# Optimization experiments

Measured on AMD Instinct MI355X. Metric: run time of the kernel, lower is better.

Reference implementation:

```python
import jax, jax.numpy as jnp
import numpy as np

HIDDEN = 4096
N_Q_HEADS = 32
N_KV_HEADS = 8
HEAD_DIM = 128
V_HEAD_DIM = 128
WINDOW = 1024
ROPE_THETA = 1000000.0
SEQ = 2048


def setup_inputs() -> dict:
    key = jax.random.key(0)
    ks = jax.random.split(key, 7)
    s = 0.02
    return {
        "hidden_states": jax.random.normal(ks[0], (SEQ, HIDDEN), dtype=jnp.float32),
        "positions": jnp.arange(SEQ, dtype=jnp.int32),
        "wq": jax.random.normal(ks[1], (HIDDEN, N_Q_HEADS * HEAD_DIM), dtype=jnp.float32) * s,
        "wk": jax.random.normal(ks[2], (HIDDEN, N_KV_HEADS * HEAD_DIM), dtype=jnp.float32) * s,
        "wv": jax.random.normal(ks[3], (HIDDEN, N_KV_HEADS * V_HEAD_DIM), dtype=jnp.float32) * s,
        "wo": jax.random.normal(ks[4], (N_Q_HEADS * V_HEAD_DIM, HIDDEN), dtype=jnp.float32) * s,
        "sink": jax.random.normal(ks[5], (N_Q_HEADS,), dtype=jnp.float32),
    }


def _apply_rope_neox(x, positions):
    # x: [S, H, D]; rotate full head_dim in neox (half-split) style
    d = x.shape[-1]
    inv_freq = 1.0 / (ROPE_THETA ** (jnp.arange(0, d, 2, dtype=jnp.float32) / d))
    freqs = positions.astype(jnp.float32)[:, None] * inv_freq[None, :]  # [S, D/2]
    cos = jnp.cos(freqs)[:, None, :]  # [S, 1, D/2]
    sin = jnp.sin(freqs)[:, None, :]
    x1, x2 = x[..., : d // 2], x[..., d // 2 :]
    return jnp.concatenate([x1 * cos - x2 * sin, x2 * cos + x1 * sin], axis=-1)


def reference(hidden_states, positions, wq, wk, wv, wo, sink):
    S = hidden_states.shape[0]
    scaling = HEAD_DIM ** -0.5
    q = (hidden_states @ wq).reshape(S, N_Q_HEADS, HEAD_DIM)
    k = (hidden_states @ wk).reshape(S, N_KV_HEADS, HEAD_DIM)
    v = (hidden_states @ wv).reshape(S, N_KV_HEADS, V_HEAD_DIM)

    q = _apply_rope_neox(q, positions)
    k = _apply_rope_neox(k, positions)

    groups = N_Q_HEADS // N_KV_HEADS
    k_rep = jnp.repeat(k, groups, axis=1)  # [S, Hq, D]
    v_rep = jnp.repeat(v, groups, axis=1)

    # [Hq, S(query), S(key)] attention scores
    scores = jnp.einsum("qhd,khd->hqk", q, k_rep) * scaling

    # causal + sliding-window mask: key j visible iff j <= i and i - j < WINDOW
    i = positions[:, None].astype(jnp.int32)
    j = positions[None, :].astype(jnp.int32)
    mask = (j <= i) & (i - j < WINDOW)  # [S, S]
    neg = jnp.finfo(scores.dtype).min
    scores = jnp.where(mask[None, :, :], scores, neg)

    # softmax with per-head attention sink logit in the denominator
    sink_l = sink[:, None, None]  # [Hq, 1, 1]
    m = jnp.maximum(scores.max(axis=-1, keepdims=True), sink_l)
    w = jnp.exp(scores - m)
    denom = w.sum(axis=-1, keepdims=True) + jnp.exp(sink_l - m)
    probs = w / denom

    attn = jnp.einsum("hqk,khd->qhd", probs, v_rep).reshape(S, N_Q_HEADS * V_HEAD_DIM)
    return attn @ wo
```

## Files before the change

kernel.cpp:

```cpp
#include <hip/hip_runtime.h>
#include <cstdint>
#include <cstddef>

typedef uint16_t u16;
typedef __bf16 bf16x8 __attribute__((ext_vector_type(8)));
typedef float f32x4 __attribute__((ext_vector_type(4)));
typedef u16 u16x8 __attribute__((ext_vector_type(8)));


__device__ __forceinline__ u16 f2bf(float f) {
    union { float f; uint32_t i; } v; v.f = f;
    uint32_t b = v.i;
    return (u16)((b + 0x7FFFu + ((b >> 16) & 1u)) >> 16);
}
__device__ __forceinline__ float bf2f(u16 u) {
    union { uint32_t i; float f; } v; v.i = ((uint32_t)u) << 16; return v.f;
}
__device__ __forceinline__ float nanfix(float x, float repl) {
    return (x == x && fabsf(x) < 1e30f) ? x : repl;
}
__device__ __forceinline__ void async16(const u16* g, u16* l) {
    __builtin_amdgcn_global_load_lds(
        (const __attribute__((address_space(1))) uint32_t*)g,
        (__attribute__((address_space(3))) uint32_t*)l, 16, 0, 0);
}

template<int N> __device__ __forceinline__ void waitvm() {
    static_assert(N >= 0 && N <= 15, "vmcnt range");
    if constexpr (N == 0)  asm volatile("s_waitcnt vmcnt(0)" ::: "memory");
    else if constexpr (N == 1)  asm volatile("s_waitcnt vmcnt(1)" ::: "memory");
    else if constexpr (N == 2)  asm volatile("s_waitcnt vmcnt(2)" ::: "memory");
    else if constexpr (N == 3)  asm volatile("s_waitcnt vmcnt(3)" ::: "memory");
    else if constexpr (N == 4)  asm volatile("s_waitcnt vmcnt(4)" ::: "memory");
    else if constexpr (N == 5)  asm volatile("s_waitcnt vmcnt(5)" ::: "memory");
    else if constexpr (N == 6)  asm volatile("s_waitcnt vmcnt(6)" ::: "memory");
    else if constexpr (N == 7)  asm volatile("s_waitcnt vmcnt(7)" ::: "memory");
    else if constexpr (N == 8)  asm volatile("s_waitcnt vmcnt(8)" ::: "memory");
    else if constexpr (N == 9)  asm volatile("s_waitcnt vmcnt(9)" ::: "memory");
    else                        asm volatile("s_waitcnt vmcnt(10)" ::: "memory");
}

__global__ void cvt_k(const float* __restrict__ in, u16* __restrict__ out) {
    const size_t i = ((size_t)blockIdx.x * 256 + threadIdx.x) * 8;
    const f32x4 a = *(const f32x4*)&in[i], b = *(const f32x4*)&in[i + 4];
    u16x8 s;
    #pragma unroll
    for (int e = 0; e < 4; e++) { s[e] = f2bf(a[e]); s[4 + e] = f2bf(b[e]); }
    *(u16x8*)&out[i] = s;
}

__global__ void cvtT_k(const float* __restrict__ in, u16* __restrict__ out,
                       int R, int C) {
    __shared__ float tile[32][33];
    const int bx = blockIdx.x * 32, by = blockIdx.y * 32;
    const int tx = threadIdx.x, ty = threadIdx.y;
    #pragma unroll
    for (int i = 0; i < 32; i += 8)
        tile[ty + i][tx] = in[(size_t)(by + ty + i) * C + (bx + tx)];
    __syncthreads();
    #pragma unroll
    for (int i = 0; i < 32; i += 8)
        out[(size_t)(bx + ty + i) * R + (by + tx)] = f2bf(tile[tx][ty + i]);
}


#define SB(g, kk, dst) async16(Bb + (size_t)((g) * 64 + rg) * 4096 + (kk) + sc, \
                               (dst) + ((g) * 64 + wave * 8) * 64)
#define SA(g, kk, dst) async16(Ab + (size_t)((g) * 32 + aro) * 4096 + (kk) + sc, \
                               (dst) + ((g) * 32 + wbA) * 64)

#define LOADA(P) do {                                                           \
    const int r0_ = wr * 128 + (2 * (P)) * 16 + lr;                             \
    const int r1_ = r0_ + 16;                                                   \
    _Pragma("unroll")                                                           \
    for (int ks = 0; ks < 2; ks++) {                                            \
        a0[ks] = *(const bf16x8*)&Ac[r0_ * 64 + (((ks * 4 + qd) ^ (r0_ & 7)) * 8)]; \
        a1[ks] = *(const bf16x8*)&Ac[r1_ * 64 + (((ks * 4 + qd) ^ (r1_ & 7)) * 8)]; \
    }                                                                           \
} while (0)

#define MFMAP(P) do {                                                           \
    __builtin_amdgcn_s_setprio(1);                                              \
    _Pragma("unroll")                                                           \
    for (int nn = 0; nn < NF; nn++)                                             \
        _Pragma("unroll")                                                       \
        for (int ks = 0; ks < 2; ks++) {                                        \
            acc[2 * (P)][nn]     = __builtin_amdgcn_mfma_f32_16x16x32_bf16(     \
                a0[ks], b[nn][ks], acc[2 * (P)][nn], 0, 0, 0);                  \
            acc[2 * (P) + 1][nn] = __builtin_amdgcn_mfma_f32_16x16x32_bf16(     \
                a1[ks], b[nn][ks], acc[2 * (P) + 1][nn], 0, 0, 0);              \
        }                                                                       \
    __builtin_amdgcn_s_setprio(0);                                              \
} while (0)

#define PHASE_SYNC() do {                                                       \
    __builtin_amdgcn_s_barrier();                                               \
    asm volatile("s_waitcnt lgkmcnt(0)" ::: "memory");                          \
    __builtin_amdgcn_sched_barrier(0);                                          \
} while (0)

#define PHASE_END() do {                                                        \
    __builtin_amdgcn_s_barrier();                                               \
    __builtin_amdgcn_sched_barrier(0);                                          \
} while (0)

template<int NF, int ISS>
__device__ __forceinline__ void tile_body(
    const u16* __restrict__ Ab, const u16* __restrict__ Bb,
    const u16* Ac, const u16* Bc, u16* An, u16* Bn, int k1,
    int wave, int lr, int qd, int wr, int wc,
    int rg, int sc, int aro, int wbA, f32x4 (&acc)[8][NF])
{
    bf16x8 b[NF][2];
    bf16x8 a0[2], a1[2];

    #pragma unroll
    for (int nn = 0; nn < NF; nn++)
        #pragma unroll
        for (int ks = 0; ks < 2; ks++) {
            const int row = wc * (16 * NF) + nn * 16 + lr;
            b[nn][ks] = *(const bf16x8*)&Bc[row * 64 + (((ks * 4 + qd) ^ (row & 7)) * 8)];
        }
    LOADA(0);
    if constexpr (ISS) {
        #pragma unroll
        for (int g = 0; g < NF; g++) SB(g, k1, Bn);
        SA(0, k1, An);
    }
    PHASE_SYNC();
    MFMAP(0);
    waitvm<ISS ? NF + 3 : 2>();
    PHASE_END();
    LOADA(1);
    if constexpr (ISS) { SA(1, k1, An); SA(2, k1, An); SA(3, k1, An); }
    PHASE_SYNC();
    MFMAP(1);
    waitvm<ISS ? NF + 5 : 1>();
    PHASE_END();
    LOADA(2);
    PHASE_SYNC();
    MFMAP(2);
    waitvm<ISS ? NF + 4 : 0>();
    PHASE_END();
    LOADA(3);
    PHASE_SYNC();
    MFMAP(3);
    if constexpr (ISS) waitvm<3>();
    PHASE_END();
}

template<int NF, int MODE>
__global__ __launch_bounds__(512, 2) void gemm256(
    const u16* __restrict__ A, const u16* __restrict__ BT,
    u16* __restrict__ qk, u16* __restrict__ vT, float* __restrict__ Cf)
{
    alignas(16) __shared__ u16 As[2][256 * 64];
    alignas(16) __shared__ u16 Bs[2][NF * 64 * 64];

    const int tid = threadIdx.x;
    const int wave = tid >> 6, lane = tid & 63;
    const int lr = lane & 15, qd = lane >> 4;
    const int wr = wave >> 2, wc = wave & 3;

    const int x = blockIdx.x & 7, bi = blockIdx.x >> 3;
    const int m0 = ((x & 1) * 4 + (bi & 3)) * 256;
    const int n0 = ((x >> 1) * 8 + (bi >> 2)) * (NF * 64);

    const u16* __restrict__ Ab = A + (size_t)m0 * 4096;
    const u16* __restrict__ Bb = BT + (size_t)n0 * 4096;

    const int rg = tid >> 3;
    const int sc = ((tid & 7) ^ (rg & 7)) * 8;
    const int aro = (rg < 32) ? rg : (96 + rg);
    const int wbA = (wave < 4) ? wave * 8 : (96 + wave * 8);

    f32x4 acc[8][NF];
    #pragma unroll
    for (int i = 0; i < 8; i++)
        #pragma unroll
        for (int j = 0; j < NF; j++) acc[i][j] = (f32x4){0.f, 0.f, 0.f, 0.f};

    #pragma unroll
    for (int g = 0; g < NF; g++) SB(g, 0, &Bs[0][0]);
    SA(0, 0, &As[0][0]); SA(1, 0, &As[0][0]); SA(2, 0, &As[0][0]); SA(3, 0, &As[0][0]);
    waitvm<3>();
    __builtin_amdgcn_s_barrier();
    __builtin_amdgcn_sched_barrier(0);

    for (int t = 0; t < 62; t += 2) {
        tile_body<NF, 1>(Ab, Bb, &As[0][0], &Bs[0][0], &As[1][0], &Bs[1][0],
                         (t + 1) * 64, wave, lr, qd, wr, wc, rg, sc, aro, wbA, acc);
        tile_body<NF, 1>(Ab, Bb, &As[1][0], &Bs[1][0], &As[0][0], &Bs[0][0],
                         (t + 2) * 64, wave, lr, qd, wr, wc, rg, sc, aro, wbA, acc);
    }
    tile_body<NF, 1>(Ab, Bb, &As[0][0], &Bs[0][0], &As[1][0], &Bs[1][0], 63 * 64,
                     wave, lr, qd, wr, wc, rg, sc, aro, wbA, acc);
    tile_body<NF, 0>(Ab, Bb, &As[1][0], &Bs[1][0], &As[0][0], &Bs[0][0], 0,
                     wave, lr, qd, wr, wc, rg, sc, aro, wbA, acc);

    #pragma unroll
    for (int i = 0; i < 8; i++)
        #pragma unroll
        for (int j = 0; j < NF; j++) {
            const int col = n0 + wc * (16 * NF) + j * 16 + lr;
            #pragma unroll
            for (int r = 0; r < 4; r++) {
                const int row = m0 + wr * 128 + i * 16 + qd * 4 + r;
                if constexpr (MODE == 0) {
                    const u16 val = f2bf(nanfix(acc[i][j][r], 1000.0f));
                    if (col < 5120) qk[(size_t)row * 5120 + col] = val;
                    else            vT[(size_t)(col - 5120) * 2048 + row] = val;
                } else {
                    Cf[(size_t)row * 4096 + col] = nanfix(acc[i][j][r], 30000.0f);
                }
            }
        }
}

#undef SB
#undef SA
#undef LOADA
#undef MFMAP
#undef PHASE_SYNC
#undef PHASE_END

__global__ void rope_k(u16* __restrict__ qk, const int* __restrict__ positions) {
    const int s = blockIdx.x;
    const int h = blockIdx.y * 4 + (threadIdx.x >> 6);
    const int t = threadIdx.x & 63;
    u16* base = qk + (size_t)s * 5120 + ((h < 32) ? h * 128 : 4096 + (h - 32) * 128);
    const float pos = (float)positions[s];
    const float freq = pos * exp2f(-(float)t * (19.931568569324174f / 64.f));
    const float c = cosf(freq), sn = sinf(freq);
    const float x1 = bf2f(base[t]), x2 = bf2f(base[t + 64]);
    base[t]      = f2bf(x1 * c - x2 * sn);
    base[t + 64] = f2bf(x2 * c + x1 * sn);
}

__global__ __launch_bounds__(256) void attn_k(
    const u16* __restrict__ qk, const u16* __restrict__ vT,
    const float* __restrict__ sink, u16* __restrict__ out)
{
    alignas(16) __shared__ u16 Ks[64 * 128];
    alignas(16) __shared__ u16 VsT[128 * 72];
    alignas(16) __shared__ u16 Ps[4][16 * 72];

    const int h = blockIdx.y, hk = h >> 2;
    const int q0 = blockIdx.x * 64;
    const int tid = threadIdx.x, wave = tid >> 6, lane = tid & 63;
    const int lr = lane & 15, qd = lane >> 4;
    const float scaling = 0.08838834764831845f;

    bf16x8 aq[4];
    #pragma unroll
    for (int kc = 0; kc < 4; kc++)
        aq[kc] = *(const bf16x8*)&qk[(size_t)(q0 + wave * 16 + lr) * 5120 + h * 128 + kc * 32 + qd * 8];

    const float sinkv = sink[h];
    float m_run[4], l_run[4];
    #pragma unroll
    for (int r = 0; r < 4; r++) { m_run[r] = sinkv; l_run[r] = 0.f; }
    f32x4 acc_o[8];
    #pragma unroll
    for (int i = 0; i < 8; i++) acc_o[i] = (f32x4){0.f, 0.f, 0.f, 0.f};

    const int jlo = (q0 - 1023) > 0 ? (q0 - 1023) : 0;
    const int t0 = jlo >> 6, t1 = q0 >> 6;

    for (int kt = t0; kt <= t1; kt++) {
        const int j0 = kt * 64;
        __syncthreads();
        #pragma unroll
        for (int p = 0; p < 4; p++) {
            const int idx = p * 256 + tid;
            const int r = idx >> 4, cs = idx & 15, c = cs ^ (r & 15);
            async16(&qk[(size_t)(j0 + r) * 5120 + 4096 + hk * 128 + c * 8],
                    Ks + (p * 256 + wave * 64) * 8);
        }
        #pragma unroll
        for (int p = 0; p < 4; p++) {
            const int idx = p * 256 + tid;
            const int vd = idx >> 3, sc2 = (idx & 7) * 8;
            const u16x8 v = *(const u16x8*)&vT[(size_t)(hk * 128 + vd) * 2048 + j0 + sc2];
            *(u16x8*)&VsT[vd * 72 + sc2] = v;
        }
        __syncthreads();

        float sv[4][4];
        #pragma unroll
        for (int nt = 0; nt < 4; nt++) {
            f32x4 s = (f32x4){0.f, 0.f, 0.f, 0.f};
            #pragma unroll
            for (int kc = 0; kc < 4; kc++) {
                const int krow = nt * 16 + lr;
                const bf16x8 bk = *(const bf16x8*)&Ks[(krow * 16 + ((kc * 4 + qd) ^ lr)) * 8];
                s = __builtin_amdgcn_mfma_f32_16x16x32_bf16(aq[kc], bk, s, 0, 0, 0);
            }
            #pragma unroll
            for (int r = 0; r < 4; r++) sv[nt][r] = s[r];
        }

        float rmax[4] = {-1e30f, -1e30f, -1e30f, -1e30f};
        #pragma unroll
        for (int nt = 0; nt < 4; nt++) {
            const int kpos = j0 + nt * 16 + lr;
            #pragma unroll
            for (int r = 0; r < 4; r++) {
                const int qpos = q0 + wave * 16 + qd * 4 + r;
                const bool ok = (kpos <= qpos) && (qpos - kpos < 1024);
                const float x = ok ? sv[nt][r] * scaling : -1e30f;
                sv[nt][r] = x;
                rmax[r] = fmaxf(rmax[r], x);
            }
        }
        #pragma unroll
        for (int off = 1; off < 16; off <<= 1)
            #pragma unroll
            for (int r = 0; r < 4; r++)
                rmax[r] = fmaxf(rmax[r], __shfl_xor(rmax[r], off, 64));

        float alpha[4], rsum[4];
        #pragma unroll
        for (int r = 0; r < 4; r++) {
            const float mnew = fmaxf(m_run[r], rmax[r]);
            alpha[r] = __expf(m_run[r] - mnew);
            m_run[r] = mnew;
            rsum[r] = 0.f;
        }
        #pragma unroll
        for (int nt = 0; nt < 4; nt++)
            #pragma unroll
            for (int r = 0; r < 4; r++) {
                const float p = __expf(sv[nt][r] - m_run[r]);
                sv[nt][r] = p;
                rsum[r] += p;
            }
        #pragma unroll
        for (int off = 1; off < 16; off <<= 1)
            #pragma unroll
            for (int r = 0; r < 4; r++)
                rsum[r] += __shfl_xor(rsum[r], off, 64);
        #pragma unroll
        for (int r = 0; r < 4; r++)
            l_run[r] = l_run[r] * alpha[r] + rsum[r];

        #pragma unroll
        for (int nt = 0; nt < 4; nt++)
            #pragma unroll
            for (int r = 0; r < 4; r++)
                Ps[wave][(qd * 4 + r) * 72 + nt * 16 + lr] = f2bf(sv[nt][r]);

        #pragma unroll
        for (int i = 0; i < 8; i++)
            #pragma unroll
            for (int r = 0; r < 4; r++) acc_o[i][r] *= alpha[r];

        __syncthreads();

        bf16x8 pa[2];
        #pragma unroll
        for (int kc = 0; kc < 2; kc++)
            pa[kc] = *(const bf16x8*)&Ps[wave][lr * 72 + kc * 32 + qd * 8];

        #pragma unroll
        for (int nt = 0; nt < 8; nt++)
            #pragma unroll
            for (int kc = 0; kc < 2; kc++) {
                const bf16x8 bv = *(const bf16x8*)&VsT[(nt * 16 + lr) * 72 + kc * 32 + qd * 8];
                acc_o[nt] = __builtin_amdgcn_mfma_f32_16x16x32_bf16(pa[kc], bv, acc_o[nt], 0, 0, 0);
            }
    }

    float invd[4];
    #pragma unroll
    for (int r = 0; r < 4; r++)
        invd[r] = 1.f / (l_run[r] + __expf(sinkv - m_run[r]));
    #pragma unroll
    for (int nt = 0; nt < 8; nt++) {
        const int col = h * 128 + nt * 16 + lr;
        #pragma unroll
        for (int r = 0; r < 4; r++) {
            const int row = q0 + wave * 16 + qd * 4 + r;
            out[(size_t)row * 4096 + col] = f2bf(nanfix(acc_o[nt][r] * invd[r], 8.0f));
        }
    }
}

extern "C" void kernel_launch(void* const* d_in, const int* in_sizes, int n_in,
                              void* d_out, int out_size, void* d_ws, size_t ws_size,
                              hipStream_t stream)
{
    (void)in_sizes; (void)n_in; (void)out_size; (void)ws_size;
    const float* hidden    = (const float*)d_in[0];
    const int*   positions = (const int*)d_in[1];
    const float* wq   = (const float*)d_in[2];
    const float* wk   = (const float*)d_in[3];
    const float* wv   = (const float*)d_in[4];
    const float* wo   = (const float*)d_in[5];
    const float* sink = (const float*)d_in[6];
    float* out = (float*)d_out;

    char* ws = (char*)d_ws;
    u16* hiddenB = (u16*)(ws);
    u16* wqkvT   = (u16*)(ws + (size_t)16777216);
    u16* qk      = (u16*)(ws + (size_t)67108864);
    u16* vT      = (u16*)(ws + (size_t)88080384);
    u16* woT     = (u16*)(ws);
    u16* attnB   = (u16*)(ws + (size_t)33554432);

    cvt_k <<<4096, 256, 0, stream>>>(hidden, hiddenB);
    cvtT_k<<<dim3(128, 128), dim3(32, 8), 0, stream>>>(wq, wqkvT, 4096, 4096);
    cvtT_k<<<dim3(32, 128),  dim3(32, 8), 0, stream>>>(wk, wqkvT + (size_t)4096 * 4096, 4096, 1024);
    cvtT_k<<<dim3(32, 128),  dim3(32, 8), 0, stream>>>(wv, wqkvT + (size_t)5120 * 4096, 4096, 1024);

    gemm256<3, 0><<<256, 512, 0, stream>>>(hiddenB, wqkvT, qk, vT, nullptr);

    cvtT_k<<<dim3(128, 128), dim3(32, 8), 0, stream>>>(wo, woT, 4096, 4096);

    rope_k<<<dim3(2048, 10), 256, 0, stream>>>(qk, positions);
    attn_k<<<dim3(32, 32), 256, 0, stream>>>(qk, vT, sink, attnB);

    gemm256<2, 1><<<256, 512, 0, stream>>>(attnB, woT, nullptr, nullptr, out);
}
```

Before: 514.6 us.

## Deepen GEMM prefetch to load tile k+2 into the current LDS buffer

Restructures the double-buffered GEMM pipeline so that, while computing tile k, the kernel issues global-to-LDS loads for tile k+2 into the same buffer as each sub-phase finishes reading it. Only the last A slice of tile k+1 is fetched into the other buffer. The prologue preloads two tiles, and the vmcnt waits are extended up to 14 outstanding loads. This aims to hide more global memory latency, at the cost of tighter reliance on the barrier ordering that makes in-place overwrite of partially consumed LDS safe.

```diff
diff --git a/kernel.cpp b/kernel.cpp
--- a/kernel.cpp
+++ b/kernel.cpp
@@ -26,7 +26,7 @@
 }
 
 template<int N> __device__ __forceinline__ void waitvm() {
-    static_assert(N >= 0 && N <= 15, "vmcnt range");
+    static_assert(N >= 0 && N <= 14, "vmcnt range");
     if constexpr (N == 0)  asm volatile("s_waitcnt vmcnt(0)" ::: "memory");
     else if constexpr (N == 1)  asm volatile("s_waitcnt vmcnt(1)" ::: "memory");
     else if constexpr (N == 2)  asm volatile("s_waitcnt vmcnt(2)" ::: "memory");
@@ -37,7 +37,11 @@
     else if constexpr (N == 7)  asm volatile("s_waitcnt vmcnt(7)" ::: "memory");
     else if constexpr (N == 8)  asm volatile("s_waitcnt vmcnt(8)" ::: "memory");
     else if constexpr (N == 9)  asm volatile("s_waitcnt vmcnt(9)" ::: "memory");
-    else                        asm volatile("s_waitcnt vmcnt(10)" ::: "memory");
+    else if constexpr (N == 10) asm volatile("s_waitcnt vmcnt(10)" ::: "memory");
+    else if constexpr (N == 11) asm volatile("s_waitcnt vmcnt(11)" ::: "memory");
+    else if constexpr (N == 12) asm volatile("s_waitcnt vmcnt(12)" ::: "memory");
+    else if constexpr (N == 13) asm volatile("s_waitcnt vmcnt(13)" ::: "memory");
+    else                        asm volatile("s_waitcnt vmcnt(14)" ::: "memory");
 }
 
 __global__ void cvt_k(const float* __restrict__ in, u16* __restrict__ out) {
@@ -107,10 +111,14 @@
 template<int NF, int ISS>
 __device__ __forceinline__ void tile_body(
     const u16* __restrict__ Ab, const u16* __restrict__ Bb,
-    const u16* Ac, const u16* Bc, u16* An, u16* Bn, int k1,
+    u16* Ac, u16* Bc, u16* Aoth, int k1, int k2,
     int wave, int lr, int qd, int wr, int wc,
     int rg, int sc, int aro, int wbA, f32x4 (&acc)[8][NF])
 {
+    constexpr int W0 = (ISS == 0) ? 2 : NF + 6;
+    constexpr int W1 = (ISS == 2) ? 2 * NF + 7 : (ISS == 1 ? NF + 5 : 1);
+    constexpr int W2 = (ISS == 2) ? 2 * NF + 6 : (ISS == 1 ? NF + 4 : 0);
+
     bf16x8 b[NF][2];
     bf16x8 a0[2], a1[2];
 
@@ -122,30 +130,33 @@
             b[nn][ks] = *(const bf16x8*)&Bc[row * 64 + (((ks * 4 + qd) ^ (row & 7)) * 8)];
         }
     LOADA(0);
-    if constexpr (ISS) {
-        #pragma unroll
-        for (int g = 0; g < NF; g++) SB(g, k1, Bn);
-        SA(0, k1, An);
+    if constexpr (ISS >= 1) SA(3, k1, Aoth);
+    PHASE_SYNC();
+    MFMAP(0);
+    waitvm<W0>();
+    PHASE_END();
+    LOADA(1);
+    if constexpr (ISS == 2) {
+        #pragma unroll
+        for (int g = 0; g < NF; g++) SB(g, k2, Bc);
+        SA(0, k2, Ac);
     }
     PHASE_SYNC();
-    MFMAP(0);
-    waitvm<ISS ? NF + 3 : 2>();
-    PHASE_END();
-    LOADA(1);
-    if constexpr (ISS) { SA(1, k1, An); SA(2, k1, An); SA(3, k1, An); }
-    PHASE_SYNC();
     MFMAP(1);
-    waitvm<ISS ? NF + 5 : 1>();
+    waitvm<W1>();
     PHASE_END();
     LOADA(2);
+    if constexpr (ISS == 2) SA(1, k2, Ac);
     PHASE_SYNC();
     MFMAP(2);
-    waitvm<ISS ? NF + 4 : 0>();
+    waitvm<W2>();
     PHASE_END();
     LOADA(3);
+    if constexpr (ISS == 2) SA(2, k2, Ac);
     PHASE_SYNC();
     MFMAP(3);
-    if constexpr (ISS) waitvm<3>();
+    if constexpr (ISS == 2) waitvm<NF + 6>();
+    else if constexpr (ISS == 1) waitvm<3>();
     PHASE_END();
 }
 
@@ -183,19 +194,24 @@
     #pragma unroll
     for (int g = 0; g < NF; g++) SB(g, 0, &Bs[0][0]);
     SA(0, 0, &As[0][0]); SA(1, 0, &As[0][0]); SA(2, 0, &As[0][0]); SA(3, 0, &As[0][0]);
-    waitvm<3>();
+    #pragma unroll
+    for (int g = 0; g < NF; g++) SB(g, 64, &Bs[1][0]);
+    SA(0, 64, &As[1][0]); SA(1, 64, &As[1][0]); SA(2, 64, &As[1][0]);
+    waitvm<NF + 6>();
     __builtin_amdgcn_s_barrier();
     __builtin_amdgcn_sched_barrier(0);
 
     for (int t = 0; t < 62; t += 2) {
-        tile_body<NF, 1>(Ab, Bb, &As[0][0], &Bs[0][0], &As[1][0], &Bs[1][0],
-                         (t + 1) * 64, wave, lr, qd, wr, wc, rg, sc, aro, wbA, acc);
-        tile_body<NF, 1>(Ab, Bb, &As[1][0], &Bs[1][0], &As[0][0], &Bs[0][0],
-                         (t + 2) * 64, wave, lr, qd, wr, wc, rg, sc, aro, wbA, acc);
+        tile_body<NF, 2>(Ab, Bb, &As[0][0], &Bs[0][0], &As[1][0],
+                         (t + 1) * 64, (t + 2) * 64,
+                         wave, lr, qd, wr, wc, rg, sc, aro, wbA, acc);
+        tile_body<NF, 2>(Ab, Bb, &As[1][0], &Bs[1][0], &As[0][0],
+                         (t + 2) * 64, (t + 3) * 64,
+                         wave, lr, qd, wr, wc, rg, sc, aro, wbA, acc);
     }
-    tile_body<NF, 1>(Ab, Bb, &As[0][0], &Bs[0][0], &As[1][0], &Bs[1][0], 63 * 64,
+    tile_body<NF, 1>(Ab, Bb, &As[0][0], &Bs[0][0], &As[1][0], 63 * 64, 0,
                      wave, lr, qd, wr, wc, rg, sc, aro, wbA, acc);
-    tile_body<NF, 0>(Ab, Bb, &As[1][0], &Bs[1][0], &As[0][0], &Bs[0][0], 0,
+    tile_body<NF, 0>(Ab, Bb, &As[1][0], &Bs[1][0], &As[0][0], 0, 0,
                      wave, lr, qd, wr, wc, rg, sc, aro, wbA, acc);
 
     #pragma unroll
```

New measurement: 535.5 us. +4.1%, slower.

## Restructure GEMM K-tile into two phases with all prefetches issued up front

Applied to the files above, without the earlier changes.

The GEMM tile body is reorganized from four phases (two A fragments each) into two phases that each load four A fragments and run larger MFMA batches. All async global-to-LDS loads for the next K tile are now issued at the start of the tile, and the vmcnt waits are adjusted to match. The main loop is also rolled into a single loop that selects buffers with a runtime odd/even flag instead of being manually unrolled by two. This cuts barrier count per tile in half but raises register pressure for A fragments, and the runtime buffer selection may add address arithmetic.

```diff
diff --git a/kernel.cpp b/kernel.cpp
--- a/kernel.cpp
+++ b/kernel.cpp
@@ -26,7 +26,7 @@
 }
 
 template<int N> __device__ __forceinline__ void waitvm() {
-    static_assert(N >= 0 && N <= 15, "vmcnt range");
+    static_assert(N >= 0 && N <= 14, "vmcnt range");
     if constexpr (N == 0)  asm volatile("s_waitcnt vmcnt(0)" ::: "memory");
     else if constexpr (N == 1)  asm volatile("s_waitcnt vmcnt(1)" ::: "memory");
     else if constexpr (N == 2)  asm volatile("s_waitcnt vmcnt(2)" ::: "memory");
@@ -37,7 +37,11 @@
     else if constexpr (N == 7)  asm volatile("s_waitcnt vmcnt(7)" ::: "memory");
     else if constexpr (N == 8)  asm volatile("s_waitcnt vmcnt(8)" ::: "memory");
     else if constexpr (N == 9)  asm volatile("s_waitcnt vmcnt(9)" ::: "memory");
-    else                        asm volatile("s_waitcnt vmcnt(10)" ::: "memory");
+    else if constexpr (N == 10) asm volatile("s_waitcnt vmcnt(10)" ::: "memory");
+    else if constexpr (N == 11) asm volatile("s_waitcnt vmcnt(11)" ::: "memory");
+    else if constexpr (N == 12) asm volatile("s_waitcnt vmcnt(12)" ::: "memory");
+    else if constexpr (N == 13) asm volatile("s_waitcnt vmcnt(13)" ::: "memory");
+    else                        asm volatile("s_waitcnt vmcnt(14)" ::: "memory");
 }
 
 __global__ void cvt_k(const float* __restrict__ in, u16* __restrict__ out) {
@@ -69,27 +73,26 @@
 #define SA(g, kk, dst) async16(Ab + (size_t)((g) * 32 + aro) * 4096 + (kk) + sc, \
                                (dst) + ((g) * 32 + wbA) * 64)
 
-#define LOADA(P) do {                                                           \
-    const int r0_ = wr * 128 + (2 * (P)) * 16 + lr;                             \
-    const int r1_ = r0_ + 16;                                                   \
+#define LOADA4(PH) do {                                                         \
     _Pragma("unroll")                                                           \
-    for (int ks = 0; ks < 2; ks++) {                                            \
-        a0[ks] = *(const bf16x8*)&Ac[r0_ * 64 + (((ks * 4 + qd) ^ (r0_ & 7)) * 8)]; \
-        a1[ks] = *(const bf16x8*)&Ac[r1_ * 64 + (((ks * 4 + qd) ^ (r1_ & 7)) * 8)]; \
+    for (int f = 0; f < 4; f++) {                                               \
+        const int row = wr * 128 + ((PH) * 4 + f) * 16 + lr;                    \
+        _Pragma("unroll")                                                       \
+        for (int ks = 0; ks < 2; ks++)                                          \
+            a[f][ks] = *(const bf16x8*)&Ac[row * 64 + (((ks * 4 + qd) ^ (row & 7)) * 8)]; \
     }                                                                           \
 } while (0)
 
-#define MFMAP(P) do {                                                           \
+#define MFMAP4(PH) do {                                                         \
     __builtin_amdgcn_s_setprio(1);                                              \
     _Pragma("unroll")                                                           \
-    for (int nn = 0; nn < NF; nn++)                                             \
+    for (int f = 0; f < 4; f++)                                                 \
         _Pragma("unroll")                                                       \
-        for (int ks = 0; ks < 2; ks++) {                                        \
-            acc[2 * (P)][nn]     = __builtin_amdgcn_mfma_f32_16x16x32_bf16(     \
-                a0[ks], b[nn][ks], acc[2 * (P)][nn], 0, 0, 0);                  \
-            acc[2 * (P) + 1][nn] = __builtin_amdgcn_mfma_f32_16x16x32_bf16(     \
-                a1[ks], b[nn][ks], acc[2 * (P) + 1][nn], 0, 0, 0);              \
-        }                                                                       \
+        for (int nn = 0; nn < NF; nn++)                                         \
+            _Pragma("unroll")                                                   \
+            for (int ks = 0; ks < 2; ks++)                                      \
+                acc[(PH) * 4 + f][nn] = __builtin_amdgcn_mfma_f32_16x16x32_bf16(\
+                    a[f][ks], b[nn][ks], acc[(PH) * 4 + f][nn], 0, 0, 0);       \
     __builtin_amdgcn_s_setprio(0);                                              \
 } while (0)
 
@@ -112,7 +115,7 @@
     int rg, int sc, int aro, int wbA, f32x4 (&acc)[8][NF])
 {
     bf16x8 b[NF][2];
-    bf16x8 a0[2], a1[2];
+    bf16x8 a[4][2];
 
     #pragma unroll
     for (int nn = 0; nn < NF; nn++)
@@ -121,31 +124,20 @@
             const int row = wc * (16 * NF) + nn * 16 + lr;
             b[nn][ks] = *(const bf16x8*)&Bc[row * 64 + (((ks * 4 + qd) ^ (row & 7)) * 8)];
         }
-    LOADA(0);
+    LOADA4(0);
     if constexpr (ISS) {
         #pragma unroll
         for (int g = 0; g < NF; g++) SB(g, k1, Bn);
-        SA(0, k1, An);
+        SA(0, k1, An); SA(1, k1, An); SA(2, k1, An); SA(3, k1, An);
     }
     PHASE_SYNC();
-    MFMAP(0);
-    waitvm<ISS ? NF + 3 : 2>();
-    PHASE_END();
-    LOADA(1);
-    if constexpr (ISS) { SA(1, k1, An); SA(2, k1, An); SA(3, k1, An); }
-    PHASE_SYNC();
-    MFMAP(1);
-    waitvm<ISS ? NF + 5 : 1>();
-    PHASE_END();
-    LOADA(2);
-    PHASE_SYNC();
-    MFMAP(2);
+    MFMAP4(0);
     waitvm<ISS ? NF + 4 : 0>();
     PHASE_END();
-    LOADA(3);
+    LOADA4(1);
     PHASE_SYNC();
-    MFMAP(3);
-    if constexpr (ISS) waitvm<3>();
+    MFMAP4(1);
+    if constexpr (ISS) waitvm<2>();
     PHASE_END();
 }
 
@@ -183,18 +175,17 @@
     #pragma unroll
     for (int g = 0; g < NF; g++) SB(g, 0, &Bs[0][0]);
     SA(0, 0, &As[0][0]); SA(1, 0, &As[0][0]); SA(2, 0, &As[0][0]); SA(3, 0, &As[0][0]);
-    waitvm<3>();
+    waitvm<2>();
     __builtin_amdgcn_s_barrier();
     __builtin_amdgcn_sched_barrier(0);
 
-    for (int t = 0; t < 62; t += 2) {
-        tile_body<NF, 1>(Ab, Bb, &As[0][0], &Bs[0][0], &As[1][0], &Bs[1][0],
+    for (int t = 0; t < 63; ++t) {
+        const bool odd = t & 1;
+        tile_body<NF, 1>(Ab, Bb,
+                         odd ? &As[1][0] : &As[0][0], odd ? &Bs[1][0] : &Bs[0][0],
+                         odd ? &As[0][0] : &As[1][0], odd ? &Bs[0][0] : &Bs[1][0],
                          (t + 1) * 64, wave, lr, qd, wr, wc, rg, sc, aro, wbA, acc);
-        tile_body<NF, 1>(Ab, Bb, &As[1][0], &Bs[1][0], &As[0][0], &Bs[0][0],
-                         (t + 2) * 64, wave, lr, qd, wr, wc, rg, sc, aro, wbA, acc);
     }
-    tile_body<NF, 1>(Ab, Bb, &As[0][0], &Bs[0][0], &As[1][0], &Bs[1][0], 63 * 64,
-                     wave, lr, qd, wr, wc, rg, sc, aro, wbA, acc);
     tile_body<NF, 0>(Ab, Bb, &As[1][0], &Bs[1][0], &As[0][0], &Bs[0][0], 0,
                      wave, lr, qd, wr, wc, rg, sc, aro, wbA, acc);
 
@@ -219,8 +210,8 @@
 
 #undef SB
 #undef SA
-#undef LOADA
-#undef MFMAP
+#undef LOADA4
+#undef MFMAP4
 #undef PHASE_SYNC
 #undef PHASE_END
 
```

Result: no change. 518.1 us (+0.7%).
